# Kernel optimization log

Measured on AMD Instinct MI355X. Metric: run time of the kernel, lower is better.

Reference implementation:

```python
import jax, jax.numpy as jnp
import numpy as np

B, T, H = 128, 500, 512  # batch, time steps, hidden size; wx has 2H features


def setup_inputs() -> dict:
    key = jax.random.key(0)
    k1, k2, k3, k4 = jax.random.split(key, 4)
    wx = jax.random.normal(k1, (B, T, 2 * H), dtype=jnp.float32)
    u = jax.random.normal(k2, (2 * H, H), dtype=jnp.float32) * 0.05  # recurrent weight
    ht = jax.random.normal(k3, (B, H), dtype=jnp.float32)
    drop_mask = jax.random.uniform(k4, (B, H), dtype=jnp.float32)
    return {"wx": wx, "u": u, "ht": ht, "drop_mask": drop_mask}


def reference(wx, u, ht, drop_mask):
    """LiGRU cell forward: sequential recurrence over time via lax.scan.

    wx: [B, T, 2H] linearly transformed input
    u:  [2H, H]    recurrent weight
    ht: [B, H]     initial hidden state
    drop_mask: [B, H] dropout mask applied to candidate at every step
    Returns (ht, zt, at, hcand) each [B, T, H].
    """
    uT = u.T  # [H, 2H]

    def step(h, wx_t):
        gates = wx_t + h @ uT              # [B, 2H]
        at, zt_pre = jnp.split(gates, 2, axis=1)
        zt = jax.nn.sigmoid(zt_pre)
        hcand = jax.nn.relu(at) * drop_mask  # act='relu'
        h_new = h * zt + (1.0 - zt) * hcand
        return h_new, (h_new, zt, at, hcand)

    wx_t_major = jnp.swapaxes(wx, 0, 1)     # [T, B, 2H]
    _, (hs, zs, ats, hcs) = jax.lax.scan(step, ht, wx_t_major)
    tr = lambda x: jnp.swapaxes(x, 0, 1)    # [T,B,H] -> [B,T,H]
    return tr(hs), tr(zs), tr(ats), tr(hcs)
```

## Files before the change

kernel.cpp:

```cpp
#include <hip/hip_runtime.h>
#include <hip/hip_fp16.h>

#define BB 128
#define TT 500
#define HH 512
#define TWOH 1024
#define KB 16

typedef _Float16 f16x8 __attribute__((ext_vector_type(8)));
typedef float f32x4 __attribute__((ext_vector_type(4)));
typedef unsigned long long u64;

#define WS_U16_HALVES (TWOH * HH)
#define HX_WORDS (8 * 2 * 16 * HH)

__global__ void prep_kernel(const float* __restrict__ u,
                            const float* __restrict__ ht,
                            __half* __restrict__ u16,
                            unsigned* __restrict__ hx) {
  int i = blockIdx.x * blockDim.x + threadIdx.x;
  if (i < WS_U16_HALVES) u16[i] = __float2half(u[i]);
  if (i < HX_WORDS) {
    int g = i >> 14, rem = i & 16383;
    int par = rem >> 13, m = (rem >> 9) & 15, k = rem & 511;
    unsigned val;
    if (par == 0) {
      int R = g * 16 + m;
      val = (unsigned)__half_as_ushort(__float2half(ht[(size_t)R * HH + k]));
    } else {
      val = 0xFFFF0000u;
    }
    hx[i] = val;
  }
}

#define TAGMASK 0xFFFF0000FFFF0000ull

__global__ __launch_bounds__(256, 1) void ligru_mfma(
    const float* __restrict__ wx, const __half* __restrict__ u16,
    const float* __restrict__ ht, const float* __restrict__ mask,
    float* __restrict__ out, unsigned* __restrict__ hx) {
  const int tid = threadIdx.x;
  const int lane = tid & 63;
  const int w = tid >> 6;
  const int l15 = lane & 15;
  const int q = lane >> 4;
  const int b = blockIdx.x;
  const int g = b >> 3;
  const int s = b & 7;
  const int row0 = g * 16;
  const int j = s * 64 + w * 16 + l15;

  __shared__ alignas(16) char hsm[2][16 * 1024];

  f16x8 bf[KB][2];
#pragma unroll
  for (int kb = 0; kb < KB; ++kb) {
    bf[kb][0] = *(const f16x8*)(u16 + (size_t)j * HH + kb * 32 + q * 8);
    bf[kb][1] = *(const f16x8*)(u16 + (size_t)(HH + j) * HH + kb * 32 + q * 8);
  }

  float hreg[4], mreg[4];
#pragma unroll
  for (int r = 0; r < 4; ++r) {
    size_t off = (size_t)(row0 + 4 * q + r) * HH + j;
    mreg[r] = mask[off];
    hreg[r] = ht[off];
  }

  const size_t BTH = (size_t)BB * TT * HH;
  float* out_h = out;
  float* out_z = out + BTH;
  float* out_a = out + 2 * BTH;
  float* out_hc = out + 3 * BTH;

  const u64* hxg = (const u64*)hx + ((size_t)g << 13);

  u64 qw[16];
#pragma unroll
  for (int pp = 0; pp < 16; ++pp)
    qw[pp] = __hip_atomic_load(hxg + pp * 256 + tid, __ATOMIC_RELAXED,
                               __HIP_MEMORY_SCOPE_AGENT);

  for (int t = 0; t < TT; ++t) {
    const int par = t & 1;

    float wxa[4], wxz[4];
#pragma unroll
    for (int r = 0; r < 4; ++r) {
      size_t base = ((size_t)(row0 + 4 * q + r) * TT + t) * TWOH + j;
      wxa[r] = wx[base];
      wxz[r] = wx[base + HH];
    }

    {
      const u64* src = hxg + par * 4096 + tid;
      const u64 tagp = ((u64)(unsigned)t << 48) | ((u64)(unsigned)t << 16);
      bool ok = true;
#pragma unroll
      for (int pp = 0; pp < 16; ++pp) ok &= ((qw[pp] & TAGMASK) == tagp);
      int bail = 0;
      while (!__all(ok)) {
        __builtin_amdgcn_s_sleep(1);
#pragma unroll
        for (int pp = 0; pp < 16; ++pp)
          qw[pp] = __hip_atomic_load(src + pp * 256, __ATOMIC_RELAXED,
                                     __HIP_MEMORY_SCOPE_AGENT);
        ok = true;
#pragma unroll
        for (int pp = 0; pp < 16; ++pp) ok &= ((qw[pp] & TAGMASK) == tagp);
        if (++bail > (1 << 15)) break;
      }
    }

    {
      char* dst = hsm[par];
#pragma unroll
      for (int pp = 0; pp < 16; ++pp) {
        unsigned d0 = (unsigned)qw[pp], d1 = (unsigned)(qw[pp] >> 32);
        unsigned pk = (d0 & 0xFFFFu) | (d1 << 16);
        *(unsigned*)(dst + ((pp * 1024 + tid * 4) ^ ((pp & 7) << 4))) = pk;
      }
    }
    __syncthreads();

    f32x4 acc0 = {0.f, 0.f, 0.f, 0.f}, acc1 = {0.f, 0.f, 0.f, 0.f};
#pragma unroll
    for (int kb = 0; kb < KB; ++kb) {
      int off = (l15 * 1024 + kb * 64 + q * 16) ^ ((l15 & 7) << 4);
      f16x8 af = *(const f16x8*)(hsm[par] + off);
      acc0 = __builtin_amdgcn_mfma_f32_16x16x32_f16(af, bf[kb][0], acc0, 0, 0, 0);
      acc1 = __builtin_amdgcn_mfma_f32_16x16x32_f16(af, bf[kb][1], acc1, 0, 0, 0);
    }

    unsigned* hd = hx + ((size_t)(g * 2 + (par ^ 1)) << 13);
    const unsigned tg = (unsigned)(t + 1) << 16;
    float atv[4], ztv[4], hcv[4];
#pragma unroll
    for (int r = 0; r < 4; ++r) {
      float at = acc0[r] + wxa[r];
      float zp = acc1[r] + wxz[r];
      float zt = 1.f / (1.f + __expf(-zp));
      float hc = fmaxf(at, 0.f) * mreg[r];
      float hn = hreg[r] * zt + (1.f - zt) * hc;
      hreg[r] = hn;
      __hip_atomic_store(hd + (4 * q + r) * HH + j,
                         tg | (unsigned)__half_as_ushort(__float2half(hn)),
                         __ATOMIC_RELAXED, __HIP_MEMORY_SCOPE_AGENT);
      atv[r] = at;
      ztv[r] = zt;
      hcv[r] = hc;
    }

    if (t + 1 < TT) {
      const u64* srcn = hxg + (par ^ 1) * 4096 + tid;
#pragma unroll
      for (int pp = 0; pp < 16; ++pp)
        qw[pp] = __hip_atomic_load(srcn + pp * 256, __ATOMIC_RELAXED,
                                   __HIP_MEMORY_SCOPE_AGENT);
    }

#pragma unroll
    for (int r = 0; r < 4; ++r) {
      size_t oi = ((size_t)(row0 + 4 * q + r) * TT + t) * HH + j;
      __builtin_nontemporal_store(hreg[r], &out_h[oi]);
      __builtin_nontemporal_store(ztv[r], &out_z[oi]);
      __builtin_nontemporal_store(atv[r], &out_a[oi]);
      __builtin_nontemporal_store(hcv[r], &out_hc[oi]);
    }
  }
}

extern "C" void kernel_launch(void* const* d_in, const int* in_sizes, int n_in,
                              void* d_out, int out_size, void* d_ws,
                              size_t ws_size, hipStream_t stream) {
  const float* wx = (const float*)d_in[0];
  const float* u = (const float*)d_in[1];
  const float* ht = (const float*)d_in[2];
  const float* mask = (const float*)d_in[3];
  float* out = (float*)d_out;

  __half* u16 = (__half*)d_ws;
  unsigned* hx = (unsigned*)(u16 + WS_U16_HALVES);

  hipLaunchKernelGGL(prep_kernel, dim3(2048), dim3(256), 0, stream, u, ht, u16,
                     hx);
  hipLaunchKernelGGL(ligru_mfma, dim3(64), dim3(256), 0, stream, wx, u16, ht,
                     mask, out, hx);
}
```

Measured before the change: 1.441 ms.

## Use 512-thread blocks covering 128 columns and prefetch next-step wx

Each block now runs 8 waves and covers 128 hidden columns instead of 64, so 32 workgroups take part in the per-step cross-block handoff instead of 64. The polled hidden-state fetch is split across twice as many threads, halving the per-thread poll registers. The wx inputs for step t+1 are loaded before waiting on step t, to hide global load latency behind the synchronization spin. Fewer CUs are used, and each block does more MFMA and store work per step.

```diff
diff --git a/kernel.cpp b/kernel.cpp
--- a/kernel.cpp
+++ b/kernel.cpp
@@ -36,7 +36,7 @@
 
 #define TAGMASK 0xFFFF0000FFFF0000ull
 
-__global__ __launch_bounds__(256, 1) void ligru_mfma(
+__global__ __launch_bounds__(512, 1) void ligru_mfma(
     const float* __restrict__ wx, const __half* __restrict__ u16,
     const float* __restrict__ ht, const float* __restrict__ mask,
     float* __restrict__ out, unsigned* __restrict__ hx) {
@@ -46,10 +46,10 @@
   const int l15 = lane & 15;
   const int q = lane >> 4;
   const int b = blockIdx.x;
-  const int g = b >> 3;
-  const int s = b & 7;
+  const int g = b & 7;
+  const int s = b >> 3;
   const int row0 = g * 16;
-  const int j = s * 64 + w * 16 + l15;
+  const int j = s * 128 + w * 16 + l15;
 
   __shared__ alignas(16) char hsm[2][16 * 1024];
 
@@ -75,22 +75,34 @@
   float* out_hc = out + 3 * BTH;
 
   const u64* hxg = (const u64*)hx + ((size_t)g << 13);
-
-  u64 qw[16];
-#pragma unroll
-  for (int pp = 0; pp < 16; ++pp)
-    qw[pp] = __hip_atomic_load(hxg + pp * 256 + tid, __ATOMIC_RELAXED,
+  const int mb = tid >> 8;
+  const int k2 = tid & 255;
+
+  u64 qw[8];
+#pragma unroll
+  for (int pp = 0; pp < 8; ++pp)
+    qw[pp] = __hip_atomic_load(hxg + (size_t)pp * 512 + tid, __ATOMIC_RELAXED,
                                __HIP_MEMORY_SCOPE_AGENT);
+
+  float wxa[4], wxz[4], wxa_n[4], wxz_n[4];
+#pragma unroll
+  for (int r = 0; r < 4; ++r) {
+    size_t base = ((size_t)(row0 + 4 * q + r) * TT + 0) * TWOH + j;
+    wxa[r] = wx[base];
+    wxz[r] = wx[base + HH];
+  }
 
   for (int t = 0; t < TT; ++t) {
     const int par = t & 1;
 
-    float wxa[4], wxz[4];
-#pragma unroll
-    for (int r = 0; r < 4; ++r) {
-      size_t base = ((size_t)(row0 + 4 * q + r) * TT + t) * TWOH + j;
-      wxa[r] = wx[base];
-      wxz[r] = wx[base + HH];
+    {
+      const int tn = (t + 1 < TT) ? t + 1 : t;
+#pragma unroll
+      for (int r = 0; r < 4; ++r) {
+        size_t base = ((size_t)(row0 + 4 * q + r) * TT + tn) * TWOH + j;
+        wxa_n[r] = wx[base];
+        wxz_n[r] = wx[base + HH];
+      }
     }
 
     {
@@ -98,17 +110,17 @@
       const u64 tagp = ((u64)(unsigned)t << 48) | ((u64)(unsigned)t << 16);
       bool ok = true;
 #pragma unroll
-      for (int pp = 0; pp < 16; ++pp) ok &= ((qw[pp] & TAGMASK) == tagp);
+      for (int pp = 0; pp < 8; ++pp) ok &= ((qw[pp] & TAGMASK) == tagp);
       int bail = 0;
       while (!__all(ok)) {
         __builtin_amdgcn_s_sleep(1);
 #pragma unroll
-        for (int pp = 0; pp < 16; ++pp)
-          qw[pp] = __hip_atomic_load(src + pp * 256, __ATOMIC_RELAXED,
+        for (int pp = 0; pp < 8; ++pp)
+          qw[pp] = __hip_atomic_load(src + (size_t)pp * 512, __ATOMIC_RELAXED,
                                      __HIP_MEMORY_SCOPE_AGENT);
         ok = true;
 #pragma unroll
-        for (int pp = 0; pp < 16; ++pp) ok &= ((qw[pp] & TAGMASK) == tagp);
+        for (int pp = 0; pp < 8; ++pp) ok &= ((qw[pp] & TAGMASK) == tagp);
         if (++bail > (1 << 15)) break;
       }
     }
@@ -116,10 +128,11 @@
     {
       char* dst = hsm[par];
 #pragma unroll
-      for (int pp = 0; pp < 16; ++pp) {
+      for (int pp = 0; pp < 8; ++pp) {
+        const int m = mb + pp * 2;
         unsigned d0 = (unsigned)qw[pp], d1 = (unsigned)(qw[pp] >> 32);
         unsigned pk = (d0 & 0xFFFFu) | (d1 << 16);
-        *(unsigned*)(dst + ((pp * 1024 + tid * 4) ^ ((pp & 7) << 4))) = pk;
+        *(unsigned*)(dst + ((m * 1024 + k2 * 4) ^ ((m & 7) << 4))) = pk;
       }
     }
     __syncthreads();
@@ -155,8 +168,8 @@
     if (t + 1 < TT) {
       const u64* srcn = hxg + (par ^ 1) * 4096 + tid;
 #pragma unroll
-      for (int pp = 0; pp < 16; ++pp)
-        qw[pp] = __hip_atomic_load(srcn + pp * 256, __ATOMIC_RELAXED,
+      for (int pp = 0; pp < 8; ++pp)
+        qw[pp] = __hip_atomic_load(srcn + (size_t)pp * 512, __ATOMIC_RELAXED,
                                    __HIP_MEMORY_SCOPE_AGENT);
     }
 
@@ -167,6 +180,12 @@
       __builtin_nontemporal_store(ztv[r], &out_z[oi]);
       __builtin_nontemporal_store(atv[r], &out_a[oi]);
       __builtin_nontemporal_store(hcv[r], &out_hc[oi]);
+    }
+
+#pragma unroll
+    for (int r = 0; r < 4; ++r) {
+      wxa[r] = wxa_n[r];
+      wxz[r] = wxz_n[r];
     }
   }
 }
@@ -185,6 +204,6 @@
 
   hipLaunchKernelGGL(prep_kernel, dim3(2048), dim3(256), 0, stream, u, ht, u16,
                      hx);
-  hipLaunchKernelGGL(ligru_mfma, dim3(64), dim3(256), 0, stream, wx, u16, ht,
+  hipLaunchKernelGGL(ligru_mfma, dim3(32), dim3(512), 0, stream, wx, u16, ht,
                      mask, out, hx);
 }
```

After: 1.949 ms. +35.2%, slower.

## Write own hidden slice to LDS directly and prefetch next-step wx

Applied to the files above, without the earlier changes.

Each block now writes its own freshly computed fp16 hidden-state slice straight into the next shared-memory buffer. The threads that cover that slice skip polling and reloading it from the global exchange buffer, which cuts global atomic traffic and spin work on the critical recurrence path. The wx inputs for step t+1 are also loaded one iteration ahead, so their latency overlaps with the wait and the MFMA work. In exchange there is more register use, and the LDS ownership mapping (tid in s*32..s*32+31) has to match the swizzled layout exactly.

```diff
diff --git a/kernel.cpp b/kernel.cpp
--- a/kernel.cpp
+++ b/kernel.cpp
@@ -51,6 +51,8 @@
   const int row0 = g * 16;
   const int j = s * 64 + w * 16 + l15;
 
+  const bool own = (tid >= s * 32) && (tid < s * 32 + 32);
+
   __shared__ alignas(16) char hsm[2][16 * 1024];
 
   f16x8 bf[KB][2];
@@ -82,38 +84,63 @@
     qw[pp] = __hip_atomic_load(hxg + pp * 256 + tid, __ATOMIC_RELAXED,
                                __HIP_MEMORY_SCOPE_AGENT);
 
+  float wxa[4], wxz[4], wxa_n[4], wxz_n[4];
+#pragma unroll
+  for (int r = 0; r < 4; ++r) {
+    size_t base = (size_t)(row0 + 4 * q + r) * TT * TWOH + j;
+    wxa[r] = wx[base];
+    wxz[r] = wx[base + HH];
+  }
+
   for (int t = 0; t < TT; ++t) {
     const int par = t & 1;
 
-    float wxa[4], wxz[4];
-#pragma unroll
-    for (int r = 0; r < 4; ++r) {
-      size_t base = ((size_t)(row0 + 4 * q + r) * TT + t) * TWOH + j;
-      wxa[r] = wx[base];
-      wxz[r] = wx[base + HH];
-    }
-
     {
+      const int tn = (t + 1 < TT) ? t + 1 : t;
+#pragma unroll
+      for (int r = 0; r < 4; ++r) {
+        size_t base = ((size_t)(row0 + 4 * q + r) * TT + tn) * TWOH + j;
+        wxa_n[r] = wx[base];
+        wxz_n[r] = wx[base + HH];
+      }
+    }
+
+    {
+      const bool skip = own && (t > 0);
       const u64* src = hxg + par * 4096 + tid;
       const u64 tagp = ((u64)(unsigned)t << 48) | ((u64)(unsigned)t << 16);
       bool ok = true;
 #pragma unroll
       for (int pp = 0; pp < 16; ++pp) ok &= ((qw[pp] & TAGMASK) == tagp);
-      int bail = 0;
-      while (!__all(ok)) {
-        __builtin_amdgcn_s_sleep(1);
-#pragma unroll
-        for (int pp = 0; pp < 16; ++pp)
-          qw[pp] = __hip_atomic_load(src + pp * 256, __ATOMIC_RELAXED,
-                                     __HIP_MEMORY_SCOPE_AGENT);
-        ok = true;
-#pragma unroll
-        for (int pp = 0; pp < 16; ++pp) ok &= ((qw[pp] & TAGMASK) == tagp);
-        if (++bail > (1 << 15)) break;
+      ok |= skip;
+      if (!__all(ok)) {
+        if (!skip) {
+#pragma unroll
+          for (int pp = 0; pp < 16; ++pp)
+            qw[pp] = __hip_atomic_load(src + pp * 256, __ATOMIC_RELAXED,
+                                       __HIP_MEMORY_SCOPE_AGENT);
+          ok = true;
+#pragma unroll
+          for (int pp = 0; pp < 16; ++pp) ok &= ((qw[pp] & TAGMASK) == tagp);
+        }
+        int bail = 0;
+        while (!__all(ok)) {
+          __builtin_amdgcn_s_sleep(1);
+          if (!skip) {
+#pragma unroll
+            for (int pp = 0; pp < 16; ++pp)
+              qw[pp] = __hip_atomic_load(src + pp * 256, __ATOMIC_RELAXED,
+                                         __HIP_MEMORY_SCOPE_AGENT);
+            ok = true;
+#pragma unroll
+            for (int pp = 0; pp < 16; ++pp) ok &= ((qw[pp] & TAGMASK) == tagp);
+          }
+          if (++bail > (1 << 15)) break;
+        }
       }
     }
 
-    {
+    if (!(own && t > 0)) {
       char* dst = hsm[par];
 #pragma unroll
       for (int pp = 0; pp < 16; ++pp) {
@@ -135,7 +162,9 @@
 
     unsigned* hd = hx + ((size_t)(g * 2 + (par ^ 1)) << 13);
     const unsigned tg = (unsigned)(t + 1) << 16;
+    char* ldst = hsm[par ^ 1];
     float atv[4], ztv[4], hcv[4];
+    __half hh[4];
 #pragma unroll
     for (int r = 0; r < 4; ++r) {
       float at = acc0[r] + wxa[r];
@@ -144,15 +173,22 @@
       float hc = fmaxf(at, 0.f) * mreg[r];
       float hn = hreg[r] * zt + (1.f - zt) * hc;
       hreg[r] = hn;
+      hh[r] = __float2half(hn);
       __hip_atomic_store(hd + (4 * q + r) * HH + j,
-                         tg | (unsigned)__half_as_ushort(__float2half(hn)),
+                         tg | (unsigned)__half_as_ushort(hh[r]),
                          __ATOMIC_RELAXED, __HIP_MEMORY_SCOPE_AGENT);
       atv[r] = at;
       ztv[r] = zt;
       hcv[r] = hc;
     }
 
-    if (t + 1 < TT) {
+#pragma unroll
+    for (int r = 0; r < 4; ++r) {
+      const int m = 4 * q + r;
+      *(__half*)(ldst + ((m * 1024 + j * 2) ^ ((m & 7) << 4))) = hh[r];
+    }
+
+    if (t + 1 < TT && !own) {
       const u64* srcn = hxg + (par ^ 1) * 4096 + tid;
 #pragma unroll
       for (int pp = 0; pp < 16; ++pp)
@@ -167,6 +203,12 @@
       __builtin_nontemporal_store(ztv[r], &out_z[oi]);
       __builtin_nontemporal_store(atv[r], &out_a[oi]);
       __builtin_nontemporal_store(hcv[r], &out_hc[oi]);
+    }
+
+#pragma unroll
+    for (int r = 0; r < 4; ++r) {
+      wxa[r] = wxa_n[r];
+      wxz[r] = wxz_n[r];
     }
   }
 }
```

Result: faster. 1.390 ms (median of 2 runs) (-3.6%).

## Poll tagged hidden-state directly into MFMA A-operand registers, drop LDS staging

Applied to the files above, without the earlier changes.

Repacks the cross-block hidden-state exchange so each 64-bit slot holds two fp16 values plus a 32-bit step tag. Each lane now polls with inline-asm dwordx4 loads laid out to match its MFMA A fragment, so the LDS staging copy and the __syncthreads are removed. The next step's wx values are prefetched one step ahead, and vmcnt waits are hand-placed so those prefetches overlap the tag check. The aim is to shorten the per-step critical path of the recurrence. In exchange it relies on inline asm cache bits (sc0 sc1) for coherence and on manual waitcnt accounting, which is fragile.

```diff
diff --git a/kernel.cpp b/kernel.cpp
--- a/kernel.cpp
+++ b/kernel.cpp
@@ -12,34 +12,58 @@
 typedef unsigned long long u64;
 
 #define WS_U16_HALVES (TWOH * HH)
-#define HX_WORDS (8 * 2 * 16 * HH)
+#define HX_QWORDS (8 * 2 * 16 * 256)
 
 __global__ void prep_kernel(const float* __restrict__ u,
                             const float* __restrict__ ht,
-                            __half* __restrict__ u16,
-                            unsigned* __restrict__ hx) {
+                            __half* __restrict__ u16, u64* __restrict__ hx) {
   int i = blockIdx.x * blockDim.x + threadIdx.x;
   if (i < WS_U16_HALVES) u16[i] = __float2half(u[i]);
-  if (i < HX_WORDS) {
-    int g = i >> 14, rem = i & 16383;
-    int par = rem >> 13, m = (rem >> 9) & 15, k = rem & 511;
-    unsigned val;
+  if (i < HX_QWORDS) {
+    int g = i >> 13, rem = i & 8191;
+    int par = rem >> 12, m = (rem >> 8) & 15, k2 = rem & 255;
+    u64 val;
     if (par == 0) {
       int R = g * 16 + m;
-      val = (unsigned)__half_as_ushort(__float2half(ht[(size_t)R * HH + k]));
+      unsigned lo =
+          (unsigned)__half_as_ushort(__float2half(ht[(size_t)R * HH + 2 * k2])) |
+          ((unsigned)__half_as_ushort(
+               __float2half(ht[(size_t)R * HH + 2 * k2 + 1]))
+           << 16);
+      val = (u64)lo;
     } else {
-      val = 0xFFFF0000u;
+      val = 0xFFFFFFFF00000000ull;
     }
     hx[i] = val;
   }
 }
 
-#define TAGMASK 0xFFFF0000FFFF0000ull
+#define ISSUE_POLL(PAR)                                                        \
+  {                                                                            \
+    const uint4* _p = (const uint4*)(hxg + (PAR) * 4096 + lbase);              \
+    _Pragma("unroll") for (int kb = 0; kb < KB; ++kb) {                        \
+      asm volatile("global_load_dwordx4 %0, %1, off sc0 sc1"                   \
+                   : "=v"(av[2 * kb])                                          \
+                   : "v"(_p + kb * 8)                                          \
+                   : "memory");                                                \
+      asm volatile("global_load_dwordx4 %0, %1, off offset:16 sc0 sc1"         \
+                   : "=v"(av[2 * kb + 1])                                      \
+                   : "v"(_p + kb * 8)                                          \
+                   : "memory");                                                \
+    }                                                                          \
+  }
+
+#define CHECK_TAGS(OK, T)                                                      \
+  {                                                                            \
+    OK = true;                                                                 \
+    _Pragma("unroll") for (int i = 0; i < 32; ++i) OK &=                       \
+        (av[i].y == (unsigned)(T)) & (av[i].w == (unsigned)(T));               \
+  }
 
 __global__ __launch_bounds__(256, 1) void ligru_mfma(
     const float* __restrict__ wx, const __half* __restrict__ u16,
     const float* __restrict__ ht, const float* __restrict__ mask,
-    float* __restrict__ out, unsigned* __restrict__ hx) {
+    float* __restrict__ out, u64* __restrict__ hx) {
   const int tid = threadIdx.x;
   const int lane = tid & 63;
   const int w = tid >> 6;
@@ -51,8 +75,6 @@
   const int row0 = g * 16;
   const int j = s * 64 + w * 16 + l15;
 
-  __shared__ alignas(16) char hsm[2][16 * 1024];
-
   f16x8 bf[KB][2];
 #pragma unroll
   for (int kb = 0; kb < KB; ++kb) {
@@ -75,66 +97,63 @@
   float* out_hc = out + 3 * BTH;
 
   const u64* hxg = (const u64*)hx + ((size_t)g << 13);
-
-  u64 qw[16];
-#pragma unroll
-  for (int pp = 0; pp < 16; ++pp)
-    qw[pp] = __hip_atomic_load(hxg + pp * 256 + tid, __ATOMIC_RELAXED,
-                               __HIP_MEMORY_SCOPE_AGENT);
+  const int lbase = l15 * 256 + q * 4;
+
+  uint4 av[32];
+
+  ISSUE_POLL(0)
+  asm volatile("s_waitcnt vmcnt(0)" ::: "memory");
+  __builtin_amdgcn_sched_barrier(0);
+
+  float wxa[4], wxz[4], wxa_n[4], wxz_n[4];
+#pragma unroll
+  for (int r = 0; r < 4; ++r) {
+    size_t base = (size_t)(row0 + 4 * q + r) * TT * TWOH + j;
+    wxa[r] = wx[base];
+    wxz[r] = wx[base + HH];
+  }
 
   for (int t = 0; t < TT; ++t) {
     const int par = t & 1;
 
-    float wxa[4], wxz[4];
-#pragma unroll
-    for (int r = 0; r < 4; ++r) {
-      size_t base = ((size_t)(row0 + 4 * q + r) * TT + t) * TWOH + j;
-      wxa[r] = wx[base];
-      wxz[r] = wx[base + HH];
-    }
-
     {
-      const u64* src = hxg + par * 4096 + tid;
-      const u64 tagp = ((u64)(unsigned)t << 48) | ((u64)(unsigned)t << 16);
-      bool ok = true;
-#pragma unroll
-      for (int pp = 0; pp < 16; ++pp) ok &= ((qw[pp] & TAGMASK) == tagp);
+      const int tn = (t + 1 < TT) ? t + 1 : t;
+#pragma unroll
+      for (int r = 0; r < 4; ++r) {
+        size_t base = ((size_t)(row0 + 4 * q + r) * TT + tn) * TWOH + j;
+        wxa_n[r] = wx[base];
+        wxz_n[r] = wx[base + HH];
+      }
+    }
+
+    {
+      asm volatile("s_waitcnt vmcnt(24)" ::: "memory");
+      __builtin_amdgcn_sched_barrier(0);
+      bool ok;
+      CHECK_TAGS(ok, t)
       int bail = 0;
-      while (!__all(ok)) {
-        __builtin_amdgcn_s_sleep(1);
-#pragma unroll
-        for (int pp = 0; pp < 16; ++pp)
-          qw[pp] = __hip_atomic_load(src + pp * 256, __ATOMIC_RELAXED,
-                                     __HIP_MEMORY_SCOPE_AGENT);
-        ok = true;
-#pragma unroll
-        for (int pp = 0; pp < 16; ++pp) ok &= ((qw[pp] & TAGMASK) == tagp);
-        if (++bail > (1 << 15)) break;
+      while (!__all(ok) && bail < (1 << 15)) {
+        if (bail) __builtin_amdgcn_s_sleep(1);
+        ISSUE_POLL(par)
+        asm volatile("s_waitcnt vmcnt(0)" ::: "memory");
+        __builtin_amdgcn_sched_barrier(0);
+        CHECK_TAGS(ok, t)
+        ++bail;
       }
     }
 
-    {
-      char* dst = hsm[par];
-#pragma unroll
-      for (int pp = 0; pp < 16; ++pp) {
-        unsigned d0 = (unsigned)qw[pp], d1 = (unsigned)(qw[pp] >> 32);
-        unsigned pk = (d0 & 0xFFFFu) | (d1 << 16);
-        *(unsigned*)(dst + ((pp * 1024 + tid * 4) ^ ((pp & 7) << 4))) = pk;
-      }
-    }
-    __syncthreads();
-
     f32x4 acc0 = {0.f, 0.f, 0.f, 0.f}, acc1 = {0.f, 0.f, 0.f, 0.f};
 #pragma unroll
     for (int kb = 0; kb < KB; ++kb) {
-      int off = (l15 * 1024 + kb * 64 + q * 16) ^ ((l15 & 7) << 4);
-      f16x8 af = *(const f16x8*)(hsm[par] + off);
+      uint4 d = {av[2 * kb].x, av[2 * kb].z, av[2 * kb + 1].x,
+                 av[2 * kb + 1].z};
+      f16x8 af = __builtin_bit_cast(f16x8, d);
       acc0 = __builtin_amdgcn_mfma_f32_16x16x32_f16(af, bf[kb][0], acc0, 0, 0, 0);
       acc1 = __builtin_amdgcn_mfma_f32_16x16x32_f16(af, bf[kb][1], acc1, 0, 0, 0);
     }
 
-    unsigned* hd = hx + ((size_t)(g * 2 + (par ^ 1)) << 13);
-    const unsigned tg = (unsigned)(t + 1) << 16;
+    u64* dstbase = hx + ((size_t)(g * 2 + (par ^ 1)) << 12);
+    const u64 tagn = (u64)(unsigned)(t + 1) << 32;
     float atv[4], ztv[4], hcv[4];
 #pragma unroll
     for (int r = 0; r < 4; ++r) {
@@ -144,20 +163,20 @@
       float hc = fmaxf(at, 0.f) * mreg[r];
       float hn = hreg[r] * zt + (1.f - zt) * hc;
       hreg[r] = hn;
-      __hip_atomic_store(hd + (4 * q + r) * HH + j,
-                         tg | (unsigned)__half_as_ushort(__float2half(hn)),
-                         __ATOMIC_RELAXED, __HIP_MEMORY_SCOPE_AGENT);
+      float hn_nbr = __shfl_xor(hn, 1);
+      if ((l15 & 1) == 0) {
+        unsigned lo = (unsigned)__half_as_ushort(__float2half(hn)) |
+                      ((unsigned)__half_as_ushort(__float2half(hn_nbr)) << 16);
+        __hip_atomic_store(dstbase + (4 * q + r) * 256 + (j >> 1), tagn | lo,
+                           __ATOMIC_RELAXED, __HIP_MEMORY_SCOPE_AGENT);
+      }
       atv[r] = at;
       ztv[r] = zt;
       hcv[r] = hc;
     }
 
     if (t + 1 < TT) {
-      const u64* srcn = hxg + (par ^ 1) * 4096 + tid;
-#pragma unroll
-      for (int pp = 0; pp < 16; ++pp)
-        qw[pp] = __hip_atomic_load(srcn + pp * 256, __ATOMIC_RELAXED,
-                                   __HIP_MEMORY_SCOPE_AGENT);
+      ISSUE_POLL(par ^ 1)
     }
 
 #pragma unroll
@@ -167,6 +186,12 @@
       __builtin_nontemporal_store(ztv[r], &out_z[oi]);
       __builtin_nontemporal_store(atv[r], &out_a[oi]);
       __builtin_nontemporal_store(hcv[r], &out_hc[oi]);
+    }
+
+#pragma unroll
+    for (int r = 0; r < 4; ++r) {
+      wxa[r] = wxa_n[r];
+      wxz[r] = wxz_n[r];
     }
   }
 }
@@ -181,7 +206,7 @@
   float* out = (float*)d_out;
 
   __half* u16 = (__half*)d_ws;
-  unsigned* hx = (unsigned*)(u16 + WS_U16_HALVES);
+  u64* hx = (u64*)(u16 + WS_U16_HALVES);
 
   hipLaunchKernelGGL(prep_kernel, dim3(2048), dim3(256), 0, stream, u, ht, u16,
                      hx);
```

Result: slower. 4.104 ms (+184.7%).
